# Kernel optimization log

Measured on AMD Instinct MI355X. Metric: run time of the kernel, lower is better.

## Reference

```python
import jax, jax.numpy as jnp
import numpy as np

B, S = 128, 72
ITER = 16
D_MODEL, D_INPUT = 1024, 512
MEM = 25
HEADS, DH = 8, 64
N_SO, N_SA = 256, 64
NUM_CLASSES = 1968
MH = 16
VOCAB, TED = 32, 128
SA_SZ = N_SA * (N_SA + 1) // 2  # 2080
SO_SZ = N_SO * (N_SO + 1) // 2  # 32896
I_A, J_A = np.triu_indices(N_SA)
I_O, J_O = np.triu_indices(N_SO)


def _ln(x, g, b):
    m = x.mean(-1, keepdims=True)
    v = ((x - m) ** 2).mean(-1, keepdims=True)
    return (x - m) / jnp.sqrt(v + 1e-5) * g + b


def _glu(x):
    a, g = jnp.split(x, 2, axis=-1)
    return a * jax.nn.sigmoid(g)


def setup_inputs():
    key = jax.random.key(0)
    ks = iter(jax.random.split(key, 32))

    def u(shape, s):
        return jax.random.uniform(next(ks), shape, jnp.float32, -s, s)

    return {
        "x": jax.random.randint(next(ks), (B, S), 0, VOCAB),
        "emb": u((VOCAB, TED), 1.0),
        "kv_w": u((TED, D_INPUT), (1.0 / TED) ** 0.5),
        "kv_b": jnp.zeros((D_INPUT,), jnp.float32),
        "kv_ln_g": jnp.ones((D_INPUT,), jnp.float32),
        "kv_ln_b": jnp.zeros((D_INPUT,), jnp.float32),
        "q_w": u((SA_SZ, D_INPUT), (1.0 / SA_SZ) ** 0.5),
        "q_b": jnp.zeros((D_INPUT,), jnp.float32),
        "in_proj_w": u((D_INPUT, 3 * D_INPUT), (1.0 / D_INPUT) ** 0.5),
        "in_proj_b": jnp.zeros((3 * D_INPUT,), jnp.float32),
        "out_proj_w": u((D_INPUT, D_INPUT), (1.0 / D_INPUT) ** 0.5),
        "out_proj_b": jnp.zeros((D_INPUT,), jnp.float32),
        "syn_w": u((D_INPUT + D_MODEL, 2 * D_MODEL), (1.0 / (D_INPUT + D_MODEL)) ** 0.5),
        "syn_b": jnp.zeros((2 * D_MODEL,), jnp.float32),
        "syn_ln_g": jnp.ones((D_MODEL,), jnp.float32),
        "syn_ln_b": jnp.zeros((D_MODEL,), jnp.float32),
        "tp1_w": u((MEM, 2 * MH, D_MODEL), 1.0 / (MEM + 2 * MH) ** 0.5),
        "tp1_b": jnp.zeros((1, D_MODEL, 2 * MH), jnp.float32),
        "tp2_w": u((MH, 2, D_MODEL), 1.0 / (MH + 2) ** 0.5),
        "tp2_b": jnp.zeros((1, D_MODEL, 2), jnp.float32),
        "start_act": u((D_MODEL,), (1.0 / D_MODEL) ** 0.5),
        "start_trace": u((D_MODEL, MEM), (1.0 / (D_MODEL + MEM)) ** 0.5),
        "decay_action": jnp.zeros((SA_SZ,), jnp.float32),
        "decay_out": jnp.zeros((SO_SZ,), jnp.float32),
        "out_w": u((SO_SZ, NUM_CLASSES), (1.0 / SO_SZ) ** 0.5),
        "out_b": jnp.zeros((NUM_CLASSES,), jnp.float32),
    }


def _forward(x, emb, kv_w, kv_b, kv_ln_g, kv_ln_b, q_w, q_b, in_proj_w, in_proj_b,
             out_proj_w, out_proj_b, syn_w, syn_b, syn_ln_g, syn_ln_b,
             tp1_w, tp1_b, tp2_w, tp2_b, start_act, start_trace,
             decay_action, decay_out, out_w, out_b):
    Bn = x.shape[0]
    # kv features: embed -> linear -> layernorm  (B,S,D_INPUT)
    kv = _ln(emb[x] @ kv_w + kv_b, kv_ln_g, kv_ln_b)
    Wq, Wk, Wv = jnp.split(in_proj_w, 3, axis=1)
    bq, bk, bv = jnp.split(in_proj_b, 3, axis=0)
    K = (kv @ Wk + bk).reshape(Bn, -1, HEADS, DH)  # (B,S,H,Dh)
    V = (kv @ Wv + bv).reshape(Bn, -1, HEADS, DH)
    # decayed running-sync coefficients (decay params clamped to [0,15])
    r_a = jnp.exp(-jnp.clip(decay_action, 0.0, 15.0))
    r_o = jnp.exp(-jnp.clip(decay_out, 0.0, 15.0))
    act0 = jnp.broadcast_to(start_act, (Bn, D_MODEL))
    trace0 = jnp.broadcast_to(start_trace, (Bn, D_MODEL, MEM))
    so0 = act0[:, :N_SO]
    a_o0 = so0[:, I_O] * so0[:, J_O]           # initial out-sync alpha
    b_o0 = jnp.ones_like(a_o0)
    a_a0 = jnp.zeros((Bn, SA_SZ), kv.dtype)    # None-init == zeros under update rule
    b_a0 = jnp.zeros((Bn, SA_SZ), kv.dtype)

    def step(carry, _):
        act, trace, a_a, b_a, a_o, b_o = carry
        # action synchronisation (last N_SA neurons, triu outer product)
        sa = act[:, -N_SA:]
        a_a = r_a * a_a + sa[:, I_A] * sa[:, J_A]
        b_a = r_a * b_a + 1.0
        sync_a = a_a / jnp.sqrt(b_a)
        # single-query multihead attention over kv
        q = sync_a @ q_w + q_b
        qh = (q @ Wq + bq).reshape(Bn, HEADS, DH)
        scores = jnp.einsum('bhd,bshd->bhs', qh, K) / (DH ** 0.5)
        attn = jax.nn.softmax(scores, axis=-1)
        o = jnp.einsum('bhs,bshd->bhd', attn, V).reshape(Bn, D_INPUT)
        o = o @ out_proj_w + out_proj_b
        # synapses: concat -> linear -> GLU -> layernorm
        pre = jnp.concatenate([o, act], axis=-1)
        state = _ln(_glu(pre @ syn_w + syn_b), syn_ln_g, syn_ln_b)
        # shift trace, append new state
        trace = jnp.concatenate([trace[:, :, 1:], state[:, :, None]], axis=-1)
        # per-neuron NLM: SuperLinear -> GLU -> SuperLinear -> GLU -> squeeze
        h = _glu(jnp.einsum('bdm,mhd->bdh', trace, tp1_w) + tp1_b)      # (B,D,MH)
        act = _glu(jnp.einsum('bdm,mhd->bdh', h, tp2_w) + tp2_b)[..., 0]  # (B,D)
        # out synchronisation (first N_SO neurons)
        so = act[:, :N_SO]
        a_o = r_o * a_o + so[:, I_O] * so[:, J_O]
        b_o = r_o * b_o + 1.0
        sync_o = a_o / jnp.sqrt(b_o)
        pred = sync_o @ out_w + out_b                                   # (B,C)
        lp = jax.nn.log_softmax(pred, axis=-1)
        ne = -jnp.sum(jnp.exp(lp) * lp, axis=-1) / jnp.log(jnp.float32(NUM_CLASSES))
        cert = jnp.stack([ne, 1.0 - ne], axis=-1)                       # (B,2)
        return (act, trace, a_a, b_a, a_o, b_o), (pred, cert)

    _, (preds, certs) = jax.lax.scan(step, (act0, trace0, a_a0, b_a0, a_o0, b_o0), None, length=ITER)
    predictions = jnp.moveaxis(preds, 0, -1)   # (B,C,ITER)
    certainties = jnp.moveaxis(certs, 0, -1)   # (B,2,ITER)
    return predictions, certainties


def reference(x, emb, kv_w, kv_b, kv_ln_g, kv_ln_b, q_w, q_b, in_proj_w, in_proj_b,
              out_proj_w, out_proj_b, syn_w, syn_b, syn_ln_g, syn_ln_b,
              tp1_w, tp1_b, tp2_w, tp2_b, start_act, start_trace,
              decay_action, decay_out, out_w, out_b):
    return _forward(x, emb, kv_w, kv_b, kv_ln_g, kv_ln_b, q_w, q_b, in_proj_w, in_proj_b,
                    out_proj_w, out_proj_b, syn_w, syn_b, syn_ln_g, syn_ln_b,
                    tp1_w, tp1_b, tp2_w, tp2_b, start_act, start_trace,
                    decay_action, decay_out, out_w, out_b)
```

## Files before the change

### kernel.cpp

```cpp
#include <hip/hip_runtime.h>
#include <math.h>

#define BB 128
#define SS 72
#define NITER 16
#define D_IN 512
#define D_MODEL 1024
#define MEMN 25
#define HEADS 8
#define DHH 64
#define N_SO 256
#define N_SA 64
#define SA_SZ 2080
#define SO_SZ 32896
#define NCLS 1968
#define TED 128
#define VOCAB 32
#define ROWS (BB*SS)
#define TRACE_SLOTS (MEMN + NITER)
#define QPAD 2176

#define BGN 64
#define BGKS 16
#define BGKLEN 2056
#define BGSTEPS 33
#define NPART 1984
#define WHLD 1984
#define WCHUNKS 124
#define SYNZ 6
#define NB_BIG 496
#define NB_Q 256
#define NB_ATTN 1024

typedef _Float16 half_t;
typedef _Float16 half8 __attribute__((ext_vector_type(8)));
typedef float f32x4v __attribute__((ext_vector_type(4)));

__device__ __forceinline__ float sigmoidf_(float x){ return 1.f/(1.f+expf(-x)); }

template<int NT>
__device__ __forceinline__ float bsumN(float v, float* red){
  int tid = threadIdx.x; red[tid] = v; __syncthreads();
#pragma unroll
  for (int s = NT/2; s > 0; s >>= 1){ if (tid < s) red[tid] += red[tid+s]; __syncthreads(); }
  float r = red[0]; __syncthreads(); return r;
}

__device__ __forceinline__ long triu_off(int n, int i){
  return (long)i*n - ((long)i*(i-1))/2;
}

__device__ __forceinline__ int swzA(int b){ return b ^ (((b>>9)&1)<<5); }

__global__ void k_conv(const float* __restrict__ src, half_t* __restrict__ dst, int n){
  int gid = blockIdx.x*256 + threadIdx.x;
  if (gid < n) dst[gid] = (half_t)src[gid];
}

#define CV0 (VOCAB*TED)
#define CV1 (CV0 + TED*D_IN)
#define CV2 (CV1 + D_IN*D_IN)
#define CV3 (CV2 + D_IN*D_IN)
#define CV4 (CV3 + D_IN*D_IN)
#define CV5 (CV4 + D_IN*D_IN)
#define CV6 (CV5 + D_IN*2048)
#define CV7 (CV6 + QPAD*D_IN)
__global__ void k_convall(const float* __restrict__ emb, const float* __restrict__ kv_w,
                          const float* __restrict__ in_proj_w,
                          const float* __restrict__ out_proj_w,
                          const float* __restrict__ syn_w, const float* __restrict__ q_w,
                          half_t* __restrict__ embh, half_t* __restrict__ kvwh,
                          half_t* __restrict__ Wkh, half_t* __restrict__ Wvh,
                          half_t* __restrict__ Wqh, half_t* __restrict__ oph,
                          half_t* __restrict__ synth, half_t* __restrict__ qwh){
  int gid = blockIdx.x*256 + threadIdx.x;
  if (gid < CV0){ embh[gid] = (half_t)emb[gid]; return; }
  if (gid < CV1){ int i = gid - CV0; kvwh[i] = (half_t)kv_w[i]; return; }
  if (gid < CV2){ int i = gid - CV1; int r = i >> 9, c = i & 511;
                  Wkh[i] = (half_t)in_proj_w[(size_t)r*1536 + 512 + c]; return; }
  if (gid < CV3){ int i = gid - CV2; int r = i >> 9, c = i & 511;
                  Wvh[i] = (half_t)in_proj_w[(size_t)r*1536 + 1024 + c]; return; }
  if (gid < CV4){ int i = gid - CV3; int r = i >> 9, c = i & 511;
                  Wqh[i] = (half_t)in_proj_w[(size_t)r*1536 + c]; return; }
  if (gid < CV5){ int i = gid - CV4; oph[i] = (half_t)out_proj_w[i]; return; }
  if (gid < CV6){ int i = gid - CV5; synth[i] = (half_t)syn_w[i]; return; }
  if (gid < CV7){ int i = gid - CV6; int r = i >> 9;
                  qwh[i] = (r < SA_SZ) ? (half_t)q_w[i] : (half_t)0.f; return; }
}

__global__ void k_convsyn(const float* __restrict__ Wf2, const float* __restrict__ syn_w,
                          half_t* __restrict__ Wsynh){
  int gid = blockIdx.x*256 + threadIdx.x;
  if (gid >= 1536*2048) return;
  Wsynh[gid] = (half_t)((gid < 512*2048) ? Wf2[gid] : syn_w[gid]);
}

__global__ void k_embed_h(const int* __restrict__ x, const half_t* __restrict__ embh,
                          half_t* __restrict__ out){
  int gid = blockIdx.x*256 + threadIdx.x;
  if (gid >= ROWS*(TED/8)) return;
  int row = gid >> 4, c0 = (gid & 15)*8;
  *(half8*)(out + (size_t)row*TED + c0) = *(const half8*)(embh + (size_t)x[row]*TED + c0);
}

__global__ void k_init_pairs(int n, int npairs, const float* __restrict__ decay,
                             int2* __restrict__ pairs, float* __restrict__ rv){
  int p = blockIdx.x*256 + threadIdx.x;
  if (p >= npairs) return;
  double nn = (double)n;
  double disc = (2.0*nn+1.0)*(2.0*nn+1.0) - 8.0*(double)p;
  int i = (int)floor(((2.0*nn+1.0) - sqrt(disc))*0.5);
  if (i < 0) i = 0; if (i > n-1) i = n-1;
  while (i+1 < n && triu_off(n, i+1) <= (long)p) i++;
  while (i > 0 && triu_off(n, i) > (long)p) i--;
  int j = i + (int)((long)p - triu_off(n, i));
  pairs[p] = make_int2(i, j);
  float dc = decay[p]; dc = fminf(fmaxf(dc, 0.f), 15.f);
  rv[p] = expf(-dc);
}

__global__ void k_init_act(const float* __restrict__ sa, float* __restrict__ act,
                           half_t* __restrict__ Ah16){
  int gid = blockIdx.x*256 + threadIdx.x;
  if (gid >= BB*D_MODEL) return;
  int b = gid >> 10, d = gid & 1023;
  float v = sa[d];
  act[gid] = v;
  Ah16[(size_t)b*1536 + 512 + d] = (half_t)v;
}

__global__ void k_zero(float* __restrict__ p, int n){
  int gid = blockIdx.x*256 + threadIdx.x;
  if (gid < n) p[gid] = 0.f;
}

__global__ void k_init_trace(const float* __restrict__ st, float* __restrict__ trace){
  int gid = blockIdx.x*256 + threadIdx.x;
  if (gid >= BB*MEMN*D_MODEL) return;
  int d = gid & 1023;
  int m = (gid >> 10) % MEMN;
  int b = (gid >> 10) / MEMN;
  trace[(size_t)b*TRACE_SLOTS*D_MODEL + (size_t)m*D_MODEL + d] = st[d*MEMN + m];
}

__global__ void k_init_ao(const float* __restrict__ sa, const int2* __restrict__ pairs,
                          float* __restrict__ ao){
  int p = blockIdx.x*256 + threadIdx.x;
  if (p >= SO_SZ) return;
  int b = blockIdx.y;
  int2 ij = pairs[p];
  ao[(size_t)b*SO_SZ + p] = sa[ij.x]*sa[ij.y];
}

__global__ void k_convw(const float* __restrict__ W, half_t* __restrict__ Wh){
  int gid = blockIdx.x*256 + threadIdx.x;
  if (gid >= SO_SZ*WCHUNKS) return;
  int row = gid / WCHUNKS, ch = gid - row*WCHUNKS;
  int c0 = ch*16;
  half_t* dst = Wh + (size_t)row*WHLD + c0;
  if (ch < 123){
    const float4* src = (const float4*)(W + (size_t)row*NCLS + c0);
    float4 f0 = src[0], f1 = src[1], f2 = src[2], f3 = src[3];
    half8 h0, h1;
    h0[0]=(half_t)f0.x; h0[1]=(half_t)f0.y; h0[2]=(half_t)f0.z; h0[3]=(half_t)f0.w;
    h0[4]=(half_t)f1.x; h0[5]=(half_t)f1.y; h0[6]=(half_t)f1.z; h0[7]=(half_t)f1.w;
    h1[0]=(half_t)f2.x; h1[1]=(half_t)f2.y; h1[2]=(half_t)f2.z; h1[3]=(half_t)f2.w;
    h1[4]=(half_t)f3.x; h1[5]=(half_t)f3.y; h1[6]=(half_t)f3.z; h1[7]=(half_t)f3.w;
    *(half8*)dst = h0; *(half8*)(dst+8) = h1;
  } else {
    half8 zz;
#pragma unroll
    for (int j = 0; j < 8; j++) zz[j] = (half_t)0.f;
    *(half8*)dst = zz; *(half8*)(dst+8) = zz;
  }
}

__global__ void k_colsumP(const float* __restrict__ vec, const float* __restrict__ W,
                          int ldw, float* __restrict__ part, int N){
  int col = blockIdx.x*256 + threadIdx.x;
  int kz = blockIdx.y;
  if (col >= N) return;
  float s = 0.f;
#pragma unroll
  for (int k = kz*32; k < kz*32 + 32; k++)
    s = fmaf(vec[k], W[(size_t)k*ldw + col], s);
  part[(size_t)kz*N + col] = s;
}

__global__ void k_colsumR(const float* __restrict__ part, const float* __restrict__ addb,
                          float* __restrict__ out, int N){
  int col = blockIdx.x*256 + threadIdx.x;
  if (col >= N) return;
  float s = addb[col];
#pragma unroll
  for (int z = 0; z < 16; z++) s += part[(size_t)z*N + col];
  out[col] = s;
}

__global__ __launch_bounds__(256)
void k_pgemm(const half_t* __restrict__ Ah, int ldah,
             const half_t* __restrict__ Wh16, int ldw, const float* __restrict__ bias,
             float* __restrict__ C, int ldc, int ksteps){
  __shared__ half_t As[2][128*64];
  __shared__ half_t Ws[2][64*66];
  const int tid = threadIdx.x;
  const int nb0 = blockIdx.x * 64;
  const int row0 = blockIdx.y * 128;
  const int l = tid & 63, wv = tid >> 6;
  const int mw = (wv >> 1) * 64, nw = (wv & 1) * 32;
  const int c = l & 15, g = l >> 4;

  f32x4v acc[4][2];
#pragma unroll
  for (int i = 0; i < 4; i++)
#pragma unroll
    for (int j2 = 0; j2 < 2; j2++)
#pragma unroll
      for (int r = 0; r < 4; r++) acc[i][j2][r] = 0.f;

  auto stage = [&](int s, int buf){
#pragma unroll
    for (int it = 0; it < 4; it++){
      int ch = tid + it*256;
      int m = ch >> 3, kl = (ch & 7)*8;
      half8 v = *(const half8*)(Ah + (size_t)(row0+m)*ldah + s*64 + kl);
      *(half8*)((char*)(&As[buf][0]) + swzA(ch*16)) = v;
    }
    {
      int k = tid >> 2, cs = (tid & 3) * 16;
      const half_t* wr = Wh16 + (size_t)(s*64 + k) * ldw + nb0 + cs;
      char* dst = (char*)(&Ws[buf][0]) + (size_t)(k*66 + cs) * 2;
      union { half8 v; unsigned int u[4]; } p0, p1;
      p0.v = *(const half8*)wr; p1.v = *(const half8*)(wr + 8);
#pragma unroll
      for (int q = 0; q < 4; q++){
        ((unsigned int*)dst)[q]        = p0.u[q];
        ((unsigned int*)(dst + 16))[q] = p1.u[q];
      }
    }
  };

  stage(0, 0);
  __syncthreads();
  for (int s = 0; s < ksteps; s++){
    int buf = s & 1;
    if (s + 1 < ksteps) stage(s+1, buf^1);
#pragma unroll
    for (int h = 0; h < 2; h++){
      half8 a8[4];
#pragma unroll
      for (int mb = 0; mb < 4; mb++)
        a8[mb] = *(const half8*)((const char*)(&As[buf][0]) +
                   swzA(((mw + mb*16 + c)*64 + h*32 + g*8)*2));
#pragma unroll
      for (int nb = 0; nb < 2; nb++){
        half8 b8;
        const half_t* wp = &Ws[buf][(h*32 + g*8)*66 + nw + nb*16 + c];
#pragma unroll
        for (int j = 0; j < 8; j++) b8[j] = wp[j*66];
#pragma unroll
        for (int mb = 0; mb < 4; mb++)
          acc[mb][nb] = __builtin_amdgcn_mfma_f32_16x16x32_f16(a8[mb], b8, acc[mb][nb], 0, 0, 0);
      }
    }
    __syncthreads();
  }
#pragma unroll
  for (int mb = 0; mb < 4; mb++)
#pragma unroll
    for (int nb = 0; nb < 2; nb++){
      int m = mw + mb*16 + g*4;
      int n = nb0 + nw + nb*16 + c;
      float bv = bias ? bias[n] : 0.f;
#pragma unroll
      for (int r = 0; r < 4; r++)
        C[(size_t)(row0 + m + r) * ldc + n] = acc[mb][nb][r] + bv;
    }
}

__global__ __launch_bounds__(256)
void k_syn16(const half_t* __restrict__ Ah, const half_t* __restrict__ Wh16,
             float* __restrict__ outp){
  __shared__ half_t As[2][128*64];
  __shared__ half_t Ws[2][64*66];
  const int tid = threadIdx.x;
  const int nb0 = blockIdx.x * 64;
  const int z = blockIdx.y;
  const int l = tid & 63, wv = tid >> 6;
  const int mw = (wv >> 1) * 64, nw = (wv & 1) * 32;
  const int c = l & 15, g = l >> 4;
  const int kbase = z * 256;

  f32x4v acc[4][2];
#pragma unroll
  for (int i = 0; i < 4; i++)
#pragma unroll
    for (int j2 = 0; j2 < 2; j2++)
#pragma unroll
      for (int r = 0; r < 4; r++) acc[i][j2][r] = 0.f;

  auto stage = [&](int s, int buf){
#pragma unroll
    for (int it = 0; it < 4; it++){
      int ch = tid + it*256;
      int m = ch >> 3, kl = (ch & 7)*8;
      half8 v = *(const half8*)(Ah + (size_t)m*1536 + kbase + s*64 + kl);
      *(half8*)((char*)(&As[buf][0]) + swzA(ch*16)) = v;
    }
    {
      int k = tid >> 2, cs = (tid & 3) * 16;
      const half_t* wr = Wh16 + (size_t)(kbase + s*64 + k) * 2048 + nb0 + cs;
      char* dst = (char*)(&Ws[buf][0]) + (size_t)(k*66 + cs) * 2;
      union { half8 v; unsigned int u[4]; } p0, p1;
      p0.v = *(const half8*)wr; p1.v = *(const half8*)(wr + 8);
#pragma unroll
      for (int q = 0; q < 4; q++){
        ((unsigned int*)dst)[q]        = p0.u[q];
        ((unsigned int*)(dst + 16))[q] = p1.u[q];
      }
    }
  };

  stage(0, 0);
  __syncthreads();
  for (int s = 0; s < 4; s++){
    int buf = s & 1;
    if (s + 1 < 4) stage(s+1, buf^1);
#pragma unroll
    for (int h = 0; h < 2; h++){
      half8 a8[4];
#pragma unroll
      for (int mb = 0; mb < 4; mb++)
        a8[mb] = *(const half8*)((const char*)(&As[buf][0]) +
                   swzA(((mw + mb*16 + c)*64 + h*32 + g*8)*2));
#pragma unroll
      for (int nb = 0; nb < 2; nb++){
        half8 b8;
        const half_t* wp = &Ws[buf][(h*32 + g*8)*66 + nw + nb*16 + c];
#pragma unroll
        for (int j = 0; j < 8; j++) b8[j] = wp[j*66];
#pragma unroll
        for (int mb = 0; mb < 4; mb++)
          acc[mb][nb] = __builtin_amdgcn_mfma_f32_16x16x32_f16(a8[mb], b8, acc[mb][nb], 0, 0, 0);
      }
    }
    __syncthreads();
  }
  float* pz = outp + (size_t)z * BB * 2048;
#pragma unroll
  for (int mb = 0; mb < 4; mb++)
#pragma unroll
    for (int nb = 0; nb < 2; nb++){
      int m = mw + mb*16 + g*4;
      int n = nb0 + nw + nb*16 + c;
#pragma unroll
      for (int r = 0; r < 4; r++)
        pz[(size_t)(m + r) * 2048 + n] = acc[mb][nb][r];
    }
}


__device__ __forceinline__ void dev_bigemm(int bx, int z, int tid,
    half_t* AsBuf, half_t* WsBuf,
    const half_t* __restrict__ Ah, const half_t* __restrict__ Wh,
    float* __restrict__ part){
  const int nb0 = bx * BGN;
  const int l = tid & 63, wv = tid >> 6;
  const int mw = (wv >> 1) * 64, nw = (wv & 1) * 32;
  const int c = l & 15, g = l >> 4;
  const int k0 = z * BGKLEN;

  f32x4v acc[4][2];
#pragma unroll
  for (int i = 0; i < 4; i++)
#pragma unroll
    for (int j2 = 0; j2 < 2; j2++)
#pragma unroll
      for (int r = 0; r < 4; r++) acc[i][j2][r] = 0.f;

  auto stage = [&](int s, int buf){
    const int kv = min(64, BGKLEN - s*64);
    half_t* As = AsBuf + buf*8192;
    half_t* Ws = WsBuf + buf*4224;
#pragma unroll
    for (int it = 0; it < 4; it++){
      int ch = tid + it*256;
      int m = ch >> 3, kg = ch & 7, kl = kg*8;
      half8 v;
      if (kl < kv) v = *(const half8*)(Ah + (size_t)m*SO_SZ + k0 + s*64 + kl);
      else {
#pragma unroll
        for (int j = 0; j < 8; j++) v[j] = (half_t)0.f;
      }
      *(half8*)((char*)As + swzA(ch*16)) = v;
    }
    {
      int k = tid >> 2, cs = (tid & 3) * 16;
      const half_t* wr = Wh + (size_t)(k0 + s*64 + k) * WHLD + nb0 + cs;
      char* dst = (char*)Ws + (size_t)(k*66 + cs) * 2;
      union { half8 v; unsigned int u[4]; } p0, p1;
      if (k < kv){ p0.v = *(const half8*)wr; p1.v = *(const half8*)(wr + 8); }
      else {
#pragma unroll
        for (int j = 0; j < 8; j++){ p0.v[j] = (half_t)0.f; p1.v[j] = (half_t)0.f; }
      }
#pragma unroll
      for (int q = 0; q < 4; q++){
        ((unsigned int*)dst)[q]        = p0.u[q];
        ((unsigned int*)(dst + 16))[q] = p1.u[q];
      }
    }
  };

  stage(0, 0);
  __syncthreads();
  for (int s = 0; s < BGSTEPS; s++){
    int buf = s & 1;
    if (s + 1 < BGSTEPS) stage(s+1, buf^1);
    half_t* As = AsBuf + buf*8192;
    half_t* Ws = WsBuf + buf*4224;
#pragma unroll
    for (int h = 0; h < 2; h++){
      half8 a8[4];
#pragma unroll
      for (int mb = 0; mb < 4; mb++)
        a8[mb] = *(const half8*)((const char*)As +
                   swzA(((mw + mb*16 + c)*64 + h*32 + g*8)*2));
#pragma unroll
      for (int nb = 0; nb < 2; nb++){
        half8 b8;
        const half_t* wp = Ws + (h*32 + g*8)*66 + nw + nb*16 + c;
#pragma unroll
        for (int j = 0; j < 8; j++) b8[j] = wp[j*66];
#pragma unroll
        for (int mb = 0; mb < 4; mb++)
          acc[mb][nb] = __builtin_amdgcn_mfma_f32_16x16x32_f16(a8[mb], b8, acc[mb][nb], 0, 0, 0);
      }
    }
    __syncthreads();
  }
  float* pz = part + (size_t)z * 128 * NPART;
#pragma unroll
  for (int mb = 0; mb < 4; mb++)
#pragma unroll
    for (int nb = 0; nb < 2; nb++){
      int m = mw + mb*16 + g*4;
      int n = nb0 + nw + nb*16 + c;
#pragma unroll
      for (int r = 0; r < 4; r++)
        pz[(size_t)(m + r) * NPART + n] = acc[mb][nb][r];
    }
}

__device__ __forceinline__ void dev_gemmq(int gx, int gy, int z, int tid, float* AsF,
    const float* __restrict__ act,
    const float* __restrict__ r_a, const int2* __restrict__ pairsA,
    const float* __restrict__ aaIn, float* __restrict__ aaOut,
    const half_t* __restrict__ Wh, float* __restrict__ qpart, int t){
  constexpr int KC = 32;
  const int col = gx*256 + tid;
  const int row0 = gy*4;
  const int kstart = z*544;
  const int kend = min(SA_SZ, kstart + 544);
  const bool writer = (gx == 0);
  float acc[4] = {0.f,0.f,0.f,0.f};
  for (int kk = kstart; kk < kend; kk += KC){
    __syncthreads();
    if (tid < 4*KC){
      int r = tid >> 5, k = tid & 31;
      int p = kk + k;
      int b = row0 + r;
      int2 ij = pairsA[p];
      const float* ab = act + (size_t)b*D_MODEL + (D_MODEL - N_SA);
      float rv = r_a[p];
      size_t idx = (size_t)b*SA_SZ + p;
      float a = fmaf(rv, aaIn[idx], ab[ij.x]*ab[ij.y]);
      if (writer) aaOut[idx] = a;
      float bb = 0.f;
      for (int i = 0; i <= t; i++) bb = fmaf(rv, bb, 1.f);
      AsF[r*KC + k] = a / sqrtf(bb);
    }
    __syncthreads();
#pragma unroll
    for (int k = 0; k < KC; k++){
      float w = (float)Wh[(size_t)(kk+k)*D_IN + col];
#pragma unroll
      for (int r = 0; r < 4; r++) acc[r] = fmaf(AsF[r*KC + k], w, acc[r]);
    }
  }
#pragma unroll
  for (int r = 0; r < 4; r++)
    qpart[(size_t)z*BB*D_IN + (size_t)(row0+r)*D_IN + col] = acc[r];
}

__device__ __forceinline__ void dev_attn(int bh, int tid,
    float* qs, float* attnv, float* red,
    const float* __restrict__ qpart, const float* __restrict__ bqf,
    const float* __restrict__ Km, const float* __restrict__ Vm,
    float* __restrict__ o, half_t* __restrict__ Ah16){
  const int b = bh >> 3, h = bh & 7;
  if (tid < DHH){
    int d = h*DHH + tid;
    float qv = bqf[d];
#pragma unroll
    for (int z = 0; z < 4; z++) qv += qpart[(size_t)z*BB*D_IN + (size_t)b*D_IN + d];
    qs[tid] = qv;
  }
  __syncthreads();
  float sc = -1e30f;
  if (tid < SS){
    const float* kp = Km + ((size_t)(b*SS+tid)*HEADS + h)*DHH;
    float d = 0.f;
#pragma unroll
    for (int i = 0; i < DHH; i++) d = fmaf(qs[i], kp[i], d);
    sc = d * 0.125f;
  }
  red[tid] = sc; __syncthreads();
  for (int s2 = 64; s2 > 0; s2 >>= 1){ if (tid < s2) red[tid] = fmaxf(red[tid], red[tid+s2]); __syncthreads(); }
  float m = red[0]; __syncthreads();
  float e = (tid < SS) ? expf(sc - m) : 0.f;
  red[tid] = e; __syncthreads();
  for (int s2 = 64; s2 > 0; s2 >>= 1){ if (tid < s2) red[tid] += red[tid+s2]; __syncthreads(); }
  float inv = 1.f / red[0]; __syncthreads();
  if (tid < SS) attnv[tid] = e * inv;
  __syncthreads();
  if (tid < DHH){
    const float* vp = Vm + ((size_t)(b*SS)*HEADS + h)*DHH + tid;
    float acc = 0.f;
    for (int s2 = 0; s2 < SS; s2++) acc = fmaf(attnv[s2], vp[(size_t)s2*D_IN], acc);
    int d = h*DHH + tid;
    o[(size_t)b*D_IN + d] = acc;
    Ah16[(size_t)b*1536 + d] = (half_t)acc;
  }
}

__device__ __forceinline__ void dev_out128(int b, int tid, float* pred, float* red,
    const float* __restrict__ part, const float* __restrict__ outb,
    float* __restrict__ dout, int t){
  float lmax = -1e30f;
  for (int c = tid; c < NCLS; c += 128){
    float s = outb[c];
    const float* pp = part + (size_t)b*NPART + c;
#pragma unroll
    for (int z = 0; z < BGKS; z++) s += pp[(size_t)z*128*NPART];
    pred[c] = s;
    dout[((size_t)b*NCLS + c)*NITER + t] = s;
    lmax = fmaxf(lmax, s);
  }
  red[tid] = lmax; __syncthreads();
  for (int s2 = 64; s2 > 0; s2 >>= 1){ if (tid < s2) red[tid] = fmaxf(red[tid], red[tid+s2]); __syncthreads(); }
  float m = red[0]; __syncthreads();
  float se = 0.f;
  for (int c = tid; c < NCLS; c += 128) se += expf(pred[c]-m);
  float Z = bsumN<128>(se, red);
  float logZ = m + logf(Z);
  float ent = 0.f;
  for (int c = tid; c < NCLS; c += 128){ float lp = pred[c]-logZ; ent += expf(lp)*lp; }
  float E = bsumN<128>(ent, red);
  if (tid == 0){
    float ne = -E * (1.f/logf((float)NCLS));
    float* cp = dout + (size_t)BB*NCLS*NITER + (size_t)b*2*NITER + t;
    cp[0]     = ne;
    cp[NITER] = 1.f - ne;
  }
}


__global__ __launch_bounds__(256)
void k_AB1(const half_t* __restrict__ sync_oh, const half_t* __restrict__ Wh,
           float* __restrict__ part,
           const float* __restrict__ act, const float* __restrict__ r_a,
           const int2* __restrict__ pairsA,
           const float* __restrict__ aaIn, float* __restrict__ aaOut,
           const half_t* __restrict__ qfwh, float* __restrict__ qpart, int t){
  __shared__ half_t AsBuf[2*8192];
  __shared__ half_t WsBuf[2*4224];
  int blk = blockIdx.x, tid = threadIdx.x;
  if (blk < NB_BIG){
    dev_bigemm(blk % 31, blk / 31, tid, AsBuf, WsBuf, sync_oh, Wh, part);
  } else {
    int i = blk - NB_BIG;
    dev_gemmq((i>>5)&1, i&31, i>>6, tid, (float*)AsBuf,
              act, r_a, pairsA, aaIn, aaOut, qfwh, qpart, t);
  }
}

__global__ __launch_bounds__(128)
void k_AB2(const float* __restrict__ qpart, const float* __restrict__ bqf,
           const float* __restrict__ Km, const float* __restrict__ Vm,
           float* __restrict__ o, half_t* __restrict__ Ah16,
           const float* __restrict__ part, const float* __restrict__ outb,
           float* __restrict__ dout, int tprev){
  __shared__ float sm[NCLS + 128];
  int blk = blockIdx.x, tid = threadIdx.x;
  if (blk < NB_ATTN){
    dev_attn(blk, tid, sm, sm + 64, sm + 136, qpart, bqf, Km, Vm, o, Ah16);
  } else {
    dev_out128(blk - NB_ATTN, tid, sm, sm + NCLS, part, outb, dout, tprev);
  }
}

__global__ void k_gemmq(const float* __restrict__ act,
                        const float* __restrict__ r_a, const int2* __restrict__ pairsA,
                        const float* __restrict__ aaIn, float* __restrict__ aaOut,
                        const half_t* __restrict__ Wh, float* __restrict__ qpart, int t){
  __shared__ float AsF[4*32];
  dev_gemmq(blockIdx.x, blockIdx.y, blockIdx.z, threadIdx.x, AsF,
            act, r_a, pairsA, aaIn, aaOut, Wh, qpart, t);
}

__global__ __launch_bounds__(128)
void k_attn(const float* __restrict__ qpart, const float* __restrict__ bqf,
            const float* __restrict__ Km, const float* __restrict__ Vm,
            float* __restrict__ o, half_t* __restrict__ Ah16){
  __shared__ float sm[264];
  dev_attn(blockIdx.x, threadIdx.x, sm, sm + 64, sm + 136, qpart, bqf, Km, Vm, o, Ah16);
}

__global__ __launch_bounds__(256)
void k_bigemm2h(const half_t* __restrict__ Ah, const half_t* __restrict__ Wh,
                float* __restrict__ part){
  __shared__ half_t AsBuf[2*8192];
  __shared__ half_t WsBuf[2*4224];
  dev_bigemm(blockIdx.x, blockIdx.y, threadIdx.x, AsBuf, WsBuf, Ah, Wh, part);
}

__global__ __launch_bounds__(128)
void k_out128(const float* __restrict__ part, const float* __restrict__ outb,
              float* __restrict__ dout, int t){
  __shared__ float sm[NCLS + 128];
  dev_out128(blockIdx.x, threadIdx.x, sm, sm + NCLS, part, outb, dout, t);
}

__global__ void k_gemm2srcZ(const float* __restrict__ A1, const float* __restrict__ A2,
                            const float* __restrict__ W1, const float* __restrict__ W2,
                            float* __restrict__ outp){
  constexpr int MB = 8, KC = 32;
  const int tid = threadIdx.x;
  const int col = blockIdx.x*256 + tid;
  const int row0 = blockIdx.y*MB;
  const int z = blockIdx.z;
  __shared__ float As[MB][KC];
  float acc[MB];
#pragma unroll
  for (int r = 0; r < MB; r++) acc[r] = 0.f;
  for (int kk = z*256; kk < z*256 + 256; kk += KC){
    __syncthreads();
    for (int idx = tid; idx < MB*KC; idx += 256){
      int r = idx / KC, k = idx % KC;
      int kg = kk + k;
      As[r][k] = (kg < D_IN) ? A1[(size_t)(row0+r)*D_IN + kg]
                             : A2[(size_t)(row0+r)*D_MODEL + kg - D_IN];
    }
    __syncthreads();
    const float* Wp = (kk < D_IN) ? W1 : W2;
#pragma unroll
    for (int k = 0; k < KC; k++){
      float w = Wp[(size_t)(kk+k)*2048 + col];
#pragma unroll
      for (int r = 0; r < MB; r++) acc[r] = fmaf(As[r][k], w, acc[r]);
    }
  }
#pragma unroll
  for (int r = 0; r < MB; r++)
    outp[(size_t)z*BB*2048 + (size_t)(row0+r)*2048 + col] = acc[r];
}

__global__ void k_ln_h(const float* __restrict__ X, const float* __restrict__ g,
                       const float* __restrict__ bta, half_t* __restrict__ Y, int D){
  const int row = blockIdx.x, tid = threadIdx.x;
  __shared__ float red[256];
  const float* xr = X + (size_t)row*D;
  float s = 0.f;
  for (int c = tid; c < D; c += 256) s += xr[c];
  float mean = bsumN<256>(s, red) / (float)D;
  float s2 = 0.f;
  for (int c = tid; c < D; c += 256){ float d = xr[c]-mean; s2 += d*d; }
  float var = bsumN<256>(s2, red) / (float)D;
  float inv = 1.f / sqrtf(var + 1e-5f);
  half_t* yr = Y + (size_t)row*D;
  for (int c = tid; c < D; c += 256) yr[c] = (half_t)((xr[c]-mean)*inv*g[c] + bta[c]);
}

__global__ void k_glu_ln(const float* __restrict__ synpart, const float* __restrict__ bias2,
                         const float* __restrict__ g, const float* __restrict__ bta,
                         float* __restrict__ traceSlot){
  const int b = blockIdx.x, tid = threadIdx.x;
  __shared__ float vals[D_MODEL];
  __shared__ float red[256];
  for (int c = tid; c < 1024; c += 256){
    float a = bias2[c], gg = bias2[c+1024];
#pragma unroll
    for (int z = 0; z < SYNZ; z++){
      const float* sp = synpart + (size_t)z*BB*2048 + (size_t)b*2048;
      a  += sp[c];
      gg += sp[c+1024];
    }
    vals[c] = a * sigmoidf_(gg);
  }
  __syncthreads();
  float s = 0.f;
  for (int c = tid; c < 1024; c += 256) s += vals[c];
  float mean = bsumN<256>(s, red) * (1.f/1024.f);
  float s2 = 0.f;
  for (int c = tid; c < 1024; c += 256){ float d = vals[c]-mean; s2 += d*d; }
  float var = bsumN<256>(s2, red) * (1.f/1024.f);
  float inv = 1.f / sqrtf(var + 1e-5f);
  float* out = traceSlot + (size_t)b*(TRACE_SLOTS*D_MODEL);
  for (int c = tid; c < 1024; c += 256) out[c] = (vals[c]-mean)*inv*g[c] + bta[c];
}

__global__ void k_neuron(const float* __restrict__ trace,
                         const float* __restrict__ tp1w, const float* __restrict__ tp1b,
                         const float* __restrict__ tp2w, const float* __restrict__ tp2b,
                         float* __restrict__ act, half_t* __restrict__ Ah16, int t){
  int gid = blockIdx.x*256 + threadIdx.x;
  if (gid >= BB*D_MODEL) return;
  int b = gid >> 10, d = gid & 1023;
  const float* tr = trace + (size_t)b*(TRACE_SLOTS*D_MODEL) + (size_t)(t+1)*D_MODEL + d;
  float trv[MEMN];
#pragma unroll
  for (int m = 0; m < MEMN; m++) trv[m] = tr[(size_t)m*D_MODEL];
  float o0 = tp2b[d*2+0], o1 = tp2b[d*2+1];
#pragma unroll
  for (int j = 0; j < 16; j++){
    const float* wpj = tp1w + (size_t)j*1024 + d;
    const float* wpg = tp1w + (size_t)(j+16)*1024 + d;
    float hj = tp1b[d*32 + j];
    float hg = tp1b[d*32 + j + 16];
#pragma unroll
    for (int m = 0; m < MEMN; m++){
      float tv = trv[m];
      hj = fmaf(tv, wpj[(size_t)m*32*1024], hj);
      hg = fmaf(tv, wpg[(size_t)m*32*1024], hg);
    }
    float hgv = hj * sigmoidf_(hg);
    o0 = fmaf(hgv, tp2w[(size_t)(j*2+0)*1024 + d], o0);
    o1 = fmaf(hgv, tp2w[(size_t)(j*2+1)*1024 + d], o1);
  }
  float v = o0 * sigmoidf_(o1);
  act[gid] = v;
  Ah16[(size_t)b*1536 + 512 + d] = (half_t)v;
}

__global__ void k_syncO(const float* __restrict__ act, const float* __restrict__ rv,
                        const int2* __restrict__ pairs, float* __restrict__ ao,
                        half_t* __restrict__ syncv, int t){
  int p = blockIdx.x*256 + threadIdx.x;
  if (p >= SO_SZ) return;
  int b = blockIdx.y;
  int2 ij = pairs[p];
  const float* ab = act + (size_t)b*D_MODEL;
  float r = rv[p];
  size_t idx = (size_t)b*SO_SZ + p;
  float a = fmaf(r, ao[idx], ab[ij.x]*ab[ij.y]);
  ao[idx] = a;
  float bb = 1.f;
  for (int i = 0; i <= t; i++) bb = fmaf(r, bb, 1.f);
  syncv[idx] = (half_t)(a / sqrtf(bb));
}

extern "C" void kernel_launch(void* const* d_in, const int* in_sizes, int n_in,
                              void* d_out, int out_size, void* d_ws, size_t ws_size,
                              hipStream_t stream){
  const int*   x           = (const int*)  d_in[0];
  const float* emb         = (const float*)d_in[1];
  const float* kv_w        = (const float*)d_in[2];
  const float* kv_b        = (const float*)d_in[3];
  const float* kv_ln_g     = (const float*)d_in[4];
  const float* kv_ln_b     = (const float*)d_in[5];
  const float* q_w         = (const float*)d_in[6];
  const float* q_b         = (const float*)d_in[7];
  const float* in_proj_w   = (const float*)d_in[8];
  const float* in_proj_b   = (const float*)d_in[9];
  const float* out_proj_w  = (const float*)d_in[10];
  const float* out_proj_b  = (const float*)d_in[11];
  const float* syn_w       = (const float*)d_in[12];
  const float* syn_b       = (const float*)d_in[13];
  const float* syn_ln_g    = (const float*)d_in[14];
  const float* syn_ln_b    = (const float*)d_in[15];
  const float* tp1_w       = (const float*)d_in[16];
  const float* tp1_b       = (const float*)d_in[17];
  const float* tp2_w       = (const float*)d_in[18];
  const float* tp2_b       = (const float*)d_in[19];
  const float* start_act   = (const float*)d_in[20];
  const float* start_trace = (const float*)d_in[21];
  const float* decay_action= (const float*)d_in[22];
  const float* decay_out   = (const float*)d_in[23];
  const float* out_w       = (const float*)d_in[24];
  const float* out_b       = (const float*)d_in[25];
  float* dout = (float*)d_out;

  float* w = (float*)d_ws;
  size_t off = 0;
  auto alloc = [&](size_t n){ n = (n + 3) & ~(size_t)3; float* p = w + off; off += n; return p; };
  float* region0 = alloc((size_t)BGKS*128*NPART);
  float* region1 = alloc((size_t)ROWS*D_IN);
  float* Kmat    = alloc((size_t)ROWS*D_IN);
  float* Vmat    = alloc((size_t)ROWS*D_IN);
  float* trace   = alloc((size_t)BB*TRACE_SLOTS*D_MODEL);
  half_t* sync_oh= (half_t*)alloc((size_t)BB*SO_SZ/2);
  float* a_aP    = alloc((size_t)2*BB*SA_SZ);
  float* act     = alloc((size_t)BB*D_MODEL);
  float* qpart   = alloc((size_t)4*BB*D_IN);
  float* obuf    = alloc((size_t)BB*D_IN);
  float* qfwPad  = alloc((size_t)QPAD*D_IN);
  float* Wf2     = alloc((size_t)D_IN*2048);
  float* bqf     = alloc(D_IN);
  float* bias2   = alloc(2048);
  float* colpart = alloc((size_t)16*2048);
  float* r_a     = alloc(SA_SZ);
  float* r_o     = alloc(SO_SZ);
  int2*  pairsA  = (int2*)alloc(2*SA_SZ);
  int2*  pairsO  = (int2*)alloc(2*SO_SZ);
  half_t* embh   = (half_t*)alloc((size_t)VOCAB*TED/2);
  half_t* kvwh   = (half_t*)alloc((size_t)TED*D_IN/2);
  half_t* Wkh    = (half_t*)alloc((size_t)D_IN*D_IN/2);
  half_t* Wvh    = (half_t*)alloc((size_t)D_IN*D_IN/2);
  half_t* Wqh    = (half_t*)alloc((size_t)D_IN*D_IN/2);
  half_t* oph    = (half_t*)alloc((size_t)D_IN*D_IN/2);
  half_t* synth  = (half_t*)alloc((size_t)D_IN*2048/2);
  half_t* qwh    = (half_t*)alloc((size_t)QPAD*D_IN/2);
  half_t* qfwh   = (half_t*)alloc((size_t)SA_SZ*D_IN/2);
  half_t* Wh     = (half_t*)alloc(((size_t)SO_SZ*WHLD)/2);
  half_t* Ah16   = (half_t*)alloc((size_t)BB*1536/2);
  half_t* Wsynh  = (half_t*)alloc((size_t)1536*2048/2);
  const bool use_syn16 = (off * sizeof(float) <= ws_size);

  half_t* embx_h = (half_t*)region0;
  half_t* kvh    = (half_t*)region0;
  float* part    = region0;
  float* synpart = region0;
  float* kvbuf = region1;
  float* a_o   = region1;

  dim3 blk(256);

  k_convall<<<(CV7+255)/256, blk, 0, stream>>>(emb, kv_w, in_proj_w, out_proj_w, syn_w, q_w,
                                               embh, kvwh, Wkh, Wvh, Wqh, oph, synth, qwh);
  k_embed_h<<<(ROWS*(TED/8)+255)/256, blk, 0, stream>>>(x, embh, embx_h);
  k_pgemm<<<dim3(8, ROWS/128), blk, 0, stream>>>(embx_h, TED, kvwh, D_IN, kv_b, kvbuf, D_IN, TED/64);
  k_ln_h<<<ROWS, blk, 0, stream>>>(kvbuf, kv_ln_g, kv_ln_b, kvh, D_IN);
  k_pgemm<<<dim3(8, ROWS/128), blk, 0, stream>>>(kvh, D_IN, Wkh, D_IN, in_proj_b+512,  Kmat, D_IN, D_IN/64);
  k_pgemm<<<dim3(8, ROWS/128), blk, 0, stream>>>(kvh, D_IN, Wvh, D_IN, in_proj_b+1024, Vmat, D_IN, D_IN/64);
  k_pgemm<<<dim3(8, QPAD/128), blk, 0, stream>>>(qwh, D_IN, Wqh, D_IN, nullptr, qfwPad, D_IN, D_IN/64);
  k_pgemm<<<dim3(32, D_IN/128), blk, 0, stream>>>(oph, D_IN, synth, 2048, nullptr, Wf2, 2048, D_IN/64);
  k_conv<<<(SA_SZ*D_IN+255)/256, blk, 0, stream>>>(qfwPad, qfwh, SA_SZ*D_IN);
  k_colsumP<<<dim3(2, 16), blk, 0, stream>>>(q_b, in_proj_w, 1536, colpart, D_IN);
  k_colsumR<<<2, blk, 0, stream>>>(colpart, in_proj_b, bqf, D_IN);
  k_colsumP<<<dim3(8, 16), blk, 0, stream>>>(out_proj_b, syn_w, 2048, colpart, 2048);
  k_colsumR<<<8, blk, 0, stream>>>(colpart, syn_b, bias2, 2048);
  k_convw<<<(SO_SZ*WCHUNKS+255)/256, blk, 0, stream>>>(out_w, Wh);
  if (use_syn16)
    k_convsyn<<<(1536*2048+255)/256, blk, 0, stream>>>(Wf2, syn_w, Wsynh);
  k_init_pairs<<<(SA_SZ+255)/256, blk, 0, stream>>>(N_SA, SA_SZ, decay_action, pairsA, r_a);
  k_init_pairs<<<(SO_SZ+255)/256, blk, 0, stream>>>(N_SO, SO_SZ, decay_out,    pairsO, r_o);
  k_init_act<<<(BB*D_MODEL+255)/256, blk, 0, stream>>>(start_act, act, Ah16);
  k_zero<<<(2*BB*SA_SZ+255)/256, blk, 0, stream>>>(a_aP, 2*BB*SA_SZ);
  k_init_trace<<<(BB*MEMN*D_MODEL+255)/256, blk, 0, stream>>>(start_trace, trace);
  k_init_ao<<<dim3((SO_SZ+255)/256, BB), blk, 0, stream>>>(start_act, pairsO, a_o);

  auto launch_syn = [&](){
    if (use_syn16)
      k_syn16<<<dim3(32, SYNZ), blk, 0, stream>>>(Ah16, Wsynh, synpart);
    else
      k_gemm2srcZ<<<dim3(8, 16, SYNZ), blk, 0, stream>>>(obuf, act, Wf2, syn_w, synpart);
  };
  auto launch_tail = [&](int t){
    k_glu_ln<<<BB, blk, 0, stream>>>(synpart, bias2, syn_ln_g, syn_ln_b,
                                     trace + (size_t)(MEMN+t)*D_MODEL);
    k_neuron<<<(BB*D_MODEL+255)/256, blk, 0, stream>>>(trace, tp1_w, tp1_b, tp2_w, tp2_b,
                                                       act, Ah16, t);
  };

  k_gemmq<<<dim3(2, 32, 4), blk, 0, stream>>>(act, r_a, pairsA,
      a_aP, a_aP + (size_t)BB*SA_SZ, qfwh, qpart, 0);
  k_attn<<<NB_ATTN, 128, 0, stream>>>(qpart, bqf, Kmat, Vmat, obuf, Ah16);
  launch_syn();
  launch_tail(0);

  for (int t = 1; t < NITER; t++){
    float* aaIn  = a_aP + (size_t)(t & 1)*BB*SA_SZ;
    float* aaOut = a_aP + (size_t)((t+1) & 1)*BB*SA_SZ;
    k_syncO<<<dim3((SO_SZ+255)/256, BB), blk, 0, stream>>>(act, r_o, pairsO, a_o, sync_oh, t-1);
    k_AB1<<<NB_BIG + NB_Q, blk, 0, stream>>>(sync_oh, Wh, part,
        act, r_a, pairsA, aaIn, aaOut, qfwh, qpart, t);
    k_AB2<<<NB_ATTN + BB, 128, 0, stream>>>(qpart, bqf, Kmat, Vmat, obuf, Ah16,
        part, out_b, dout, t-1);
    launch_syn();
    launch_tail(t);
  }

  k_syncO<<<dim3((SO_SZ+255)/256, BB), blk, 0, stream>>>(act, r_o, pairsO, a_o, sync_oh, NITER-1);
  k_bigemm2h<<<dim3(31, BGKS), blk, 0, stream>>>(sync_oh, Wh, part);
  k_out128<<<BB, 128, 0, stream>>>(part, out_b, dout, NITER-1);
}
```

Measured before the change: 2.636 ms.

## Software-pipeline output sync computation into the big GEMM kernel with double buffering

Moves the k_syncO work into k_AB1 as extra blocks so the output-sync vector for step t-1 is computed while the big output GEMM consumes the sync vector from step t-2. The sync_oh buffer becomes double-buffered, and the output/certainty stage lags by one extra iteration, with a drained tail at the end. This removes one kernel launch per iteration and overlaps the memory-bound sync update with the GEMM. In exchange it needs an extra workspace buffer, moves synpart out of region0, and adds a grid-stride loop with integer division per element.

```diff
diff --git a/kernel.cpp b/kernel.cpp
--- a/kernel.cpp
+++ b/kernel.cpp
@@ -30,6 +30,7 @@
 #define SYNZ 6
 #define NB_BIG 496
 #define NB_Q 256
+#define NB_SYNCO 1024
 #define NB_ATTN 1024
 
 typedef _Float16 half_t;
@@ -493,6 +494,26 @@
     qpart[(size_t)z*BB*D_IN + (size_t)(row0+r)*D_IN + col] = acc[r];
 }
 
+__device__ __forceinline__ void dev_syncO(int blk, int nblk, int tid,
+    const float* __restrict__ act, const float* __restrict__ rv,
+    const int2* __restrict__ pairs, float* __restrict__ ao,
+    half_t* __restrict__ syncv, int t){
+  for (int base = blk*256; base < BB*SO_SZ; base += nblk*256){
+    int idx = base + tid;
+    if (idx >= BB*SO_SZ) break;
+    int b = idx / SO_SZ;
+    int p = idx - b*SO_SZ;
+    int2 ij = pairs[p];
+    const float* ab = act + (size_t)b*D_MODEL;
+    float r = rv[p];
+    float a = fmaf(r, ao[idx], ab[ij.x]*ab[ij.y]);
+    ao[idx] = a;
+    float bb = 1.f;
+    for (int i = 0; i <= t; i++) bb = fmaf(r, bb, 1.f);
+    syncv[idx] = (half_t)(a / sqrtf(bb));
+  }
+}
+
 __device__ __forceinline__ void dev_attn(int bh, int tid,
     float* qs, float* attnv, float* red,
     const float* __restrict__ qpart, const float* __restrict__ bqf,
@@ -567,21 +588,26 @@
 
 
 __global__ __launch_bounds__(256)
-void k_AB1(const half_t* __restrict__ sync_oh, const half_t* __restrict__ Wh,
+void k_AB1(int nbig,
+           const half_t* __restrict__ soRead, const half_t* __restrict__ Wh,
            float* __restrict__ part,
            const float* __restrict__ act, const float* __restrict__ r_a,
            const int2* __restrict__ pairsA,
            const float* __restrict__ aaIn, float* __restrict__ aaOut,
-           const half_t* __restrict__ qfwh, float* __restrict__ qpart, int t){
+           const half_t* __restrict__ qfwh, float* __restrict__ qpart, int t,
+           const float* __restrict__ r_o, const int2* __restrict__ pairsO,
+           float* __restrict__ a_o, half_t* __restrict__ soWrite){
   __shared__ half_t AsBuf[2*8192];
   __shared__ half_t WsBuf[2*4224];
   int blk = blockIdx.x, tid = threadIdx.x;
-  if (blk < NB_BIG){
-    dev_bigemm(blk % 31, blk / 31, tid, AsBuf, WsBuf, sync_oh, Wh, part);
-  } else {
-    int i = blk - NB_BIG;
+  if (blk < nbig){
+    dev_bigemm(blk % 31, blk / 31, tid, AsBuf, WsBuf, soRead, Wh, part);
+  } else if (blk < nbig + NB_Q){
+    int i = blk - nbig;
     dev_gemmq((i>>5)&1, i&31, i>>6, tid, (float*)AsBuf,
               act, r_a, pairsA, aaIn, aaOut, qfwh, qpart, t);
+  } else {
+    dev_syncO(blk - nbig - NB_Q, NB_SYNCO, tid, act, r_o, pairsO, a_o, soWrite, t-1);
   }
 }
 
@@ -630,6 +656,12 @@
               float* __restrict__ dout, int t){
   __shared__ float sm[NCLS + 128];
   dev_out128(blockIdx.x, threadIdx.x, sm, sm + NCLS, part, outb, dout, t);
+}
+
+__global__ void k_syncO(const float* __restrict__ act, const float* __restrict__ rv,
+                        const int2* __restrict__ pairs, float* __restrict__ ao,
+                        half_t* __restrict__ syncv, int t){
+  dev_syncO(blockIdx.x, NB_SYNCO, threadIdx.x, act, rv, pairs, ao, syncv, t);
 }
 
 __global__ void k_gemm2srcZ(const float* __restrict__ A1, const float* __restrict__ A2,
@@ -741,23 +773,6 @@
   float v = o0 * sigmoidf_(o1);
   act[gid] = v;
   Ah16[(size_t)b*1536 + 512 + d] = (half_t)v;
-}
-
-__global__ void k_syncO(const float* __restrict__ act, const float* __restrict__ rv,
-                        const int2* __restrict__ pairs, float* __restrict__ ao,
-                        half_t* __restrict__ syncv, int t){
-  int p = blockIdx.x*256 + threadIdx.x;
-  if (p >= SO_SZ) return;
-  int b = blockIdx.y;
-  int2 ij = pairs[p];
-  const float* ab = act + (size_t)b*D_MODEL;
-  float r = rv[p];
-  size_t idx = (size_t)b*SO_SZ + p;
-  float a = fmaf(r, ao[idx], ab[ij.x]*ab[ij.y]);
-  ao[idx] = a;
-  float bb = 1.f;
-  for (int i = 0; i <= t; i++) bb = fmaf(r, bb, 1.f);
-  syncv[idx] = (half_t)(a / sqrtf(bb));
 }
 
 extern "C" void kernel_launch(void* const* d_in, const int* in_sizes, int n_in,
@@ -795,11 +810,12 @@
   size_t off = 0;
   auto alloc = [&](size_t n){ n = (n + 3) & ~(size_t)3; float* p = w + off; off += n; return p; };
   float* region0 = alloc((size_t)BGKS*128*NPART);
+  float* synpart = alloc((size_t)SYNZ*BB*2048);
   float* region1 = alloc((size_t)ROWS*D_IN);
   float* Kmat    = alloc((size_t)ROWS*D_IN);
   float* Vmat    = alloc((size_t)ROWS*D_IN);
   float* trace   = alloc((size_t)BB*TRACE_SLOTS*D_MODEL);
-  half_t* sync_oh= (half_t*)alloc((size_t)BB*SO_SZ/2);
+  half_t* sync_ohP = (half_t*)alloc((size_t)BB*SO_SZ);
   float* a_aP    = alloc((size_t)2*BB*SA_SZ);
   float* act     = alloc((size_t)BB*D_MODEL);
   float* qpart   = alloc((size_t)4*BB*D_IN);
@@ -830,9 +846,10 @@
   half_t* embx_h = (half_t*)region0;
   half_t* kvh    = (half_t*)region0;
   float* part    = region0;
-  float* synpart = region0;
   float* kvbuf = region1;
   float* a_o   = region1;
+  half_t* so0 = sync_ohP;
+  half_t* so1 = sync_ohP + (size_t)BB*SO_SZ;
 
   dim3 blk(256);
 
@@ -872,6 +889,7 @@
     k_neuron<<<(BB*D_MODEL+255)/256, blk, 0, stream>>>(trace, tp1_w, tp1_b, tp2_w, tp2_b,
                                                        act, Ah16, t);
   };
+  auto soBuf = [&](int t){ return (t & 1) ? so1 : so0; };
 
   k_gemmq<<<dim3(2, 32, 4), blk, 0, stream>>>(act, r_a, pairsA,
       a_aP, a_aP + (size_t)BB*SA_SZ, qfwh, qpart, 0);
@@ -879,19 +897,32 @@
   launch_syn();
   launch_tail(0);
 
-  for (int t = 1; t < NITER; t++){
+  {
+    float* aaIn  = a_aP + (size_t)BB*SA_SZ;
+    float* aaOut = a_aP;
+    k_AB1<<<NB_Q + NB_SYNCO, blk, 0, stream>>>(0, nullptr, Wh, part,
+        act, r_a, pairsA, aaIn, aaOut, qfwh, qpart, 1,
+        r_o, pairsO, a_o, soBuf(0));
+    k_attn<<<NB_ATTN, 128, 0, stream>>>(qpart, bqf, Kmat, Vmat, obuf, Ah16);
+    launch_syn();
+    launch_tail(1);
+  }
+
+  for (int t = 2; t < NITER; t++){
     float* aaIn  = a_aP + (size_t)(t & 1)*BB*SA_SZ;
     float* aaOut = a_aP + (size_t)((t+1) & 1)*BB*SA_SZ;
-    k_syncO<<<dim3((SO_SZ+255)/256, BB), blk, 0, stream>>>(act, r_o, pairsO, a_o, sync_oh, t-1);
-    k_AB1<<<NB_BIG + NB_Q, blk, 0, stream>>>(sync_oh, Wh, part,
-        act, r_a, pairsA, aaIn, aaOut, qfwh, qpart, t);
+    k_AB1<<<NB_BIG + NB_Q + NB_SYNCO, blk, 0, stream>>>(NB_BIG, soBuf(t-2), Wh, part,
+        act, r_a, pairsA, aaIn, aaOut, qfwh, qpart, t,
+        r_o, pairsO, a_o, soBuf(t-1));
     k_AB2<<<NB_ATTN + BB, 128, 0, stream>>>(qpart, bqf, Kmat, Vmat, obuf, Ah16,
-        part, out_b, dout, t-1);
+        part, out_b, dout, t-2);
     launch_syn();
     launch_tail(t);
   }
 
-  k_syncO<<<dim3((SO_SZ+255)/256, BB), blk, 0, stream>>>(act, r_o, pairsO, a_o, sync_oh, NITER-1);
-  k_bigemm2h<<<dim3(31, BGKS), blk, 0, stream>>>(sync_oh, Wh, part);
-  k_out128<<<BB, 128, 0, stream>>>(part, out_b, dout, NITER-1);
-}
+  k_bigemm2h<<<dim3(31, BGKS), blk, 0, stream>>>(soBuf(14), Wh, part);
+  k_out128<<<BB, 128, 0, stream>>>(part, out_b, dout, 14);
+  k_syncO<<<NB_SYNCO, blk, 0, stream>>>(act, r_o, pairsO, a_o, soBuf(15), 15);
+  k_bigemm2h<<<dim3(31, BGKS), blk, 0, stream>>>(soBuf(15), Wh, part);
+  k_out128<<<BB, 128, 0, stream>>>(part, out_b, dout, 15);
+}
```

Result: no change. 2.685 ms (+1.9%).
